# Optimization experiments

Measured on AMD Instinct MI355X. Metric: run time of the kernel, lower is better.

Reference implementation:

```python
import jax, jax.numpy as jnp
import numpy as np

DIM = 768
NUM_HEADS = 12
HEAD_DIM = DIM // NUM_HEADS
SCALE = HEAD_DIM ** -0.5
B, N = 4, 2048


def setup_inputs() -> dict:
    key = jax.random.key(0)
    k1, k2, k3 = jax.random.split(key, 3)
    x = jax.random.normal(k1, (B, N, DIM), dtype=jnp.float32)
    W_qk = jax.random.normal(k2, (2 * DIM, DIM), dtype=jnp.float32) * (DIM ** -0.5)
    b_qk = jax.random.normal(k3, (2 * DIM,), dtype=jnp.float32) * 0.02
    return {"x": x, "W_qk": W_qk, "b_qk": b_qk}


def reference(x, W_qk, b_qk):
    Bb, Nn, C = x.shape
    # qk projection: [B,N,2C] -> [B,N,2,H,D] -> q,k each [B,H,N,D]
    qk = x @ W_qk.T + b_qk
    qk = qk.reshape(Bb, Nn, 2, NUM_HEADS, HEAD_DIM).transpose(2, 0, 3, 1, 4)
    q, k = qk[0], qk[1]
    # attention scores [B,H,N,N]
    attn = jnp.einsum("bhnd,bhmd->bhnm", q, k) * SCALE
    attn = jax.nn.softmax(attn, axis=-1)
    # mean over heads, then per-query diagonal -> [B,N]
    attn_weights = jnp.diagonal(attn.mean(axis=1), axis1=-2, axis2=-1)
    return attn_weights
```

## Files before the change

### kernel.cpp

```cpp
#include <hip/hip_runtime.h>
#include <math.h>


#define B_ 4
#define N_ 2048
#define H_ 12
#define D_ 64
#define C_ 768
#define TWO_C 1536
#define QSCALE 0.18033688011112043f

typedef _Float16 half8 __attribute__((ext_vector_type(8)));
typedef _Float16 half4 __attribute__((ext_vector_type(4)));
typedef float floatx4 __attribute__((ext_vector_type(4)));

#if __has_builtin(__builtin_amdgcn_exp2f)
#define EXP2(x) __builtin_amdgcn_exp2f(x)
#else
#define EXP2(x) exp2f(x)
#endif

__device__ __forceinline__ void gload_lds16(const _Float16* g, _Float16* l) {
  __builtin_amdgcn_global_load_lds(
      (const __attribute__((address_space(1))) void*)g,
      (__attribute__((address_space(3))) void*)l, 16, 0, 0);
}

#define NX4 1572864
#define NW4 294912
__global__ __launch_bounds__(256) void conv_kernel(const float* __restrict__ x,
                                                   const float* __restrict__ W,
                                                   _Float16* __restrict__ xh,
                                                   _Float16* __restrict__ wh,
                                                   float* __restrict__ outz) {
  int i = blockIdx.x * 256 + threadIdx.x;
  if (i < 2048) {
    float4 z; z.x = 0.f; z.y = 0.f; z.z = 0.f; z.w = 0.f;
    ((float4*)outz)[i] = z;
  }
  const float* in;
  _Float16* out;
  int idx;
  if (i < NX4) {
    in = x; out = xh; idx = i;
  } else if (i < NX4 + NW4) {
    in = W; out = wh; idx = i - NX4;
  } else {
    return;
  }
  float4 v = ((const float4*)in)[idx];
  half4 o;
  o[0] = (_Float16)v.x; o[1] = (_Float16)v.y;
  o[2] = (_Float16)v.z; o[3] = (_Float16)v.w;
  ((half4*)out)[idx] = o;
}

__global__ __launch_bounds__(256) void proj_kernel(
    const _Float16* __restrict__ xh, const _Float16* __restrict__ wh,
    const float* __restrict__ bias, _Float16* __restrict__ qh,
    _Float16* __restrict__ kh) {
  __shared__ _Float16 As[3][128 * 32];
  __shared__ _Float16 Bs[3][128 * 32];
  const int t = threadIdx.x;
  const int l = t & 63;
  const int w = t >> 6;
  const int wr = w >> 1, wc = w & 1;

  int lin = blockIdx.y * 12 + blockIdx.x;
  int swz = (lin & 7) * 96 + (lin >> 3);
  const int bm = (swz / 12) * 128;
  const int bc = (swz % 12) * 128;

  const int srow = l >> 2;
  const int schunk = (l & 3) ^ ((l >> 3) & 3);

  floatx4 acc[4][4] = {};

#define PSTAGE(KT)                                                          \
  {                                                                         \
    const int sl_ = (KT) % 3;                                               \
    const int k0_ = (KT) * 32;                                              \
    _Pragma("unroll") for (int i_ = 0; i_ < 2; ++i_) {                      \
      int rb_ = w * 32 + i_ * 16;                                           \
      gload_lds16(xh + (size_t)(bm + rb_ + srow) * C_ + k0_ + schunk * 8,   \
                  As[sl_] + rb_ * 32);                                      \
      gload_lds16(wh + (size_t)(bc + rb_ + srow) * C_ + k0_ + schunk * 8,   \
                  Bs[sl_] + rb_ * 32);                                      \
    }                                                                       \
  }

#define PITER(KT, VMASM, DO_STAGE)                                          \
  {                                                                         \
    asm volatile(VMASM ::: "memory");                                       \
    __builtin_amdgcn_s_barrier();                                           \
    asm volatile("" ::: "memory");                                          \
    const int sl_ = (KT) % 3;                                               \
    const _Float16* Ap_ = As[sl_];                                          \
    const _Float16* Bp_ = Bs[sl_];                                          \
    half8 af[4], bf[4];                                                     \
    _Pragma("unroll") for (int fr = 0; fr < 4; ++fr) {                      \
      int row = wr * 64 + fr * 16 + (l & 15);                               \
      int ch = (l >> 4) ^ ((row >> 1) & 3);                                 \
      af[fr] = *(const half8*)(Ap_ + row * 32 + ch * 8);                    \
    }                                                                       \
    _Pragma("unroll") for (int fc = 0; fc < 4; ++fc) {                      \
      int row = wc * 64 + fc * 16 + (l & 15);                               \
      int ch = (l >> 4) ^ ((row >> 1) & 3);                                 \
      bf[fc] = *(const half8*)(Bp_ + row * 32 + ch * 8);                    \
    }                                                                       \
    if (DO_STAGE) PSTAGE((KT) + 2);                                         \
    _Pragma("unroll") for (int fr = 0; fr < 4; ++fr)                        \
        _Pragma("unroll") for (int fc = 0; fc < 4; ++fc) acc[fr][fc] =      \
        __builtin_amdgcn_mfma_f32_16x16x32_f16(af[fr], bf[fc],              \
                                               acc[fr][fc], 0, 0, 0);       \
  }

  PSTAGE(0);
  PSTAGE(1);
  for (int kt = 0; kt < 22; ++kt) PITER(kt, "s_waitcnt vmcnt(4)", true);
  PITER(22, "s_waitcnt vmcnt(4)", false);
  PITER(23, "s_waitcnt vmcnt(0)", false);
#undef PITER
#undef PSTAGE

#pragma unroll
  for (int fr = 0; fr < 4; ++fr) {
#pragma unroll
    for (int fc = 0; fc < 4; ++fc) {
#pragma unroll
      for (int j = 0; j < 4; ++j) {
        int m = bm + wr * 64 + fr * 16 + ((l >> 4) << 2) + j;
        int c = bc + wc * 64 + fc * 16 + (l & 15);
        float v = acc[fr][fc][j] + bias[c];
        int b = m >> 11, n = m & (N_ - 1);
        int cc = (c < C_) ? c : c - C_;
        if (c < C_) v *= QSCALE;
        int hh = cc >> 6, d = cc & 63;
        _Float16* dst = (c < C_) ? qh : kh;
        dst[((((size_t)b * H_ + hh) * N_ + n) << 6) + d] = (_Float16)v;
      }
    }
  }
}

__global__ __launch_bounds__(256) void attn_kernel(
    const _Float16* __restrict__ qh, const _Float16* __restrict__ kh,
    float* __restrict__ out) {
  __shared__ _Float16 ks[4][64 * 64];
  const int t = threadIdx.x;
  const int l = t & 63;
  const int w = t >> 6;

  int lin = blockIdx.x;
  int swz = (lin & 7) * 192 + (lin >> 3);
  const int qt = swz & 31;
  const int h = (swz >> 5) % 12;
  const int b = swz / 384;

  const _Float16* qb = qh + (((size_t)(b * H_ + h) * N_ + qt * 64) << 6);
  const _Float16* kb = kh + (((size_t)(b * H_ + h) * N_) << 6);

  half8 qf[4][2];
#pragma unroll
  for (int fr = 0; fr < 4; ++fr)
#pragma unroll
    for (int kd = 0; kd < 2; ++kd)
      qf[fr][kd] = *(const half8*)(qb + (size_t)(fr * 16 + (l & 15)) * 64 +
                                   kd * 32 + (l >> 4) * 8);

  const int lin0 = w * 64 + l;
  const int row0 = lin0 >> 3, slot0 = lin0 & 7;
  const int soff0 = row0 * 64 + (slot0 ^ (row0 & 7)) * 8;
  const int lin1 = lin0 + 256;
  const int row1 = lin1 >> 3, slot1 = lin1 & 7;
  const int soff1 = row1 * 64 + (slot1 ^ (row1 & 7)) * 8;

#define STAGE(KT)                                                   \
  {                                                                 \
    const _Float16* kp_ = kb + (size_t)(KT) * 4096;                 \
    _Float16* ld_ = ks[(KT) & 3];                                   \
    gload_lds16(kp_ + soff0, ld_ + w * 512);                        \
    gload_lds16(kp_ + soff1, ld_ + w * 512 + 2048);                 \
  }

  const int frow = w * 16 + (l & 15);
  const int koff0 = frow * 64 + (((l >> 4) + 0) ^ (l & 7)) * 8;
  const int koff1 = frow * 64 + (((l >> 4) + 4) ^ (l & 7)) * 8;

  floatx4 lsum[4] = {};
  float ed[4] = {0.f, 0.f, 0.f, 0.f};

  STAGE(0);
  STAGE(1);
  STAGE(2);

#define ITER(KT, VMASM, DO_STAGE)                                             \
  {                                                                           \
    asm volatile(VMASM ::: "memory");                                         \
    __builtin_amdgcn_s_barrier();                                             \
    asm volatile("" ::: "memory");                                            \
    const _Float16* bufp = ks[(KT) & 3];                                      \
    half8 kf0 = *(const half8*)(bufp + koff0);                                \
    half8 kf1 = *(const half8*)(bufp + koff1);                                \
    if (DO_STAGE) STAGE((KT) + 3);                                            \
    floatx4 acc[4] = {};                                                      \
    _Pragma("unroll") for (int fr = 0; fr < 4; ++fr) {                        \
      acc[fr] = __builtin_amdgcn_mfma_f32_16x16x32_f16(qf[fr][0], kf0,        \
                                                       acc[fr], 0, 0, 0);     \
      acc[fr] = __builtin_amdgcn_mfma_f32_16x16x32_f16(qf[fr][1], kf1,        \
                                                       acc[fr], 0, 0, 0);     \
    }                                                                         \
    _Pragma("unroll") for (int fr = 0; fr < 4; ++fr) {                        \
      floatx4 ev;                                                             \
      _Pragma("unroll") for (int j = 0; j < 4; ++j) ev[j] = EXP2(acc[fr][j]); \
      lsum[fr] += ev;                          \
    }                                                                         \
    if ((KT) == qt) {                                                         \
      _Pragma("unroll") for (int fr = 0; fr < 4; ++fr)                        \
          _Pragma("unroll") for (int j = 0; j < 4; ++j) {                     \
        if (fr == w && (l & 15) == (((l >> 4) << 2) + j))                     \
          ed[j] = EXP2(acc[fr][j]);                                           \
      }                                                                       \
    }                                                                         \
  }

  for (int kt = 0; kt < 29; ++kt) ITER(kt, "s_waitcnt vmcnt(4)", true);
  ITER(29, "s_waitcnt vmcnt(4)", false);
  ITER(30, "s_waitcnt vmcnt(2)", false);
  ITER(31, "s_waitcnt vmcnt(0)", false);
#undef ITER
#undef STAGE

#pragma unroll
  for (int fr = 0; fr < 4; ++fr)
#pragma unroll
    for (int j = 0; j < 4; ++j)
#pragma unroll
      for (int m = 1; m < 16; m <<= 1)
        lsum[fr][j] += __shfl_xor(lsum[fr][j], m, 16);
#pragma unroll
  for (int j = 0; j < 4; ++j)
#pragma unroll
    for (int m = 1; m < 16; m <<= 1) ed[j] += __shfl_xor(ed[j], m, 16);

  __builtin_amdgcn_s_barrier();
  float* red = (float*)ks[0];
  float* edl = red + 256;
  if ((l & 15) == 0) {
#pragma unroll
    for (int fr = 0; fr < 4; ++fr)
#pragma unroll
      for (int j = 0; j < 4; ++j)
        red[w * 64 + fr * 16 + ((l >> 4) << 2) + j] = lsum[fr][j];
#pragma unroll
    for (int j = 0; j < 4; ++j) edl[w * 16 + ((l >> 4) << 2) + j] = ed[j];
  }
  __syncthreads();

  if (t < 64) {
    float ls = red[t] + red[64 + t] + red[128 + t] + red[192 + t];
    atomicAdd(out + (size_t)b * N_ + qt * 64 + t,
              edl[t] / ls * (1.0f / (float)H_));
  }
}

extern "C" void kernel_launch(void* const* d_in, const int* in_sizes, int n_in,
                              void* d_out, int out_size, void* d_ws,
                              size_t ws_size, hipStream_t stream) {
  const float* x = (const float*)d_in[0];
  const float* W = (const float*)d_in[1];
  const float* bias = (const float*)d_in[2];
  float* out = (float*)d_out;

  char* ws = (char*)d_ws;
  _Float16* xh = (_Float16*)ws;
  _Float16* wh = (_Float16*)(ws + 12582912);
  _Float16* qh = (_Float16*)(ws + 14942208);
  _Float16* kh = (_Float16*)(ws + 27525120);

  conv_kernel<<<(NX4 + NW4 + 255) / 256, 256, 0, stream>>>(x, W, xh, wh, out);
  proj_kernel<<<dim3(TWO_C / 128, 8192 / 128), 256, 0, stream>>>(xh, wh, bias,
                                                                 qh, kh);
  attn_kernel<<<N_ / 64 * H_ * B_, 256, 0, stream>>>(qh, kh, out);
}
```

Baseline: 81.70 us.

## Split key-tile loop across two wave groups in 512-thread attention blocks

The attention kernel now runs 8 waves per block instead of 4. Each pipeline step stages a pair of 64-row K tiles, and waves 0-3 and 4-7 each take one tile of the pair, so the serial loop drops from 32 steps to 16 and there are half as many barriers per tile. The row-sum reduction now combines partials from all 8 waves, and only the wave group that holds the diagonal tile writes the diagonal exponentials. In exchange, Q fragments are loaded twice per block, LDS per block doubles to 64KB, and the barrier before reusing the staging buffer for the reduction is removed.

```diff
diff --git a/kernel.cpp b/kernel.cpp
--- a/kernel.cpp
+++ b/kernel.cpp
@@ -143,13 +143,15 @@
   }
 }
 
-__global__ __launch_bounds__(256) void attn_kernel(
+__global__ __launch_bounds__(512) void attn_kernel(
     const _Float16* __restrict__ qh, const _Float16* __restrict__ kh,
     float* __restrict__ out) {
-  __shared__ _Float16 ks[4][64 * 64];
+  __shared__ _Float16 ks[4][2][4096];
   const int t = threadIdx.x;
   const int l = t & 63;
   const int w = t >> 6;
+  const int wg = w & 3;
+  const int ts = w >> 2;
 
   int lin = blockIdx.x;
   int swz = (lin & 7) * 192 + (lin >> 3);
@@ -168,41 +170,34 @@
       qf[fr][kd] = *(const half8*)(qb + (size_t)(fr * 16 + (l & 15)) * 64 +
                                    kd * 32 + (l >> 4) * 8);
 
-  const int lin0 = w * 64 + l;
-  const int row0 = lin0 >> 3, slot0 = lin0 & 7;
-  const int soff0 = row0 * 64 + (slot0 ^ (row0 & 7)) * 8;
-  const int lin1 = lin0 + 256;
-  const int row1 = lin1 >> 3, slot1 = lin1 & 7;
-  const int soff1 = row1 * 64 + (slot1 ^ (row1 & 7)) * 8;
-
-#define STAGE(KT)                                                   \
-  {                                                                 \
-    const _Float16* kp_ = kb + (size_t)(KT) * 4096;                 \
-    _Float16* ld_ = ks[(KT) & 3];                                   \
-    gload_lds16(kp_ + soff0, ld_ + w * 512);                        \
-    gload_lds16(kp_ + soff1, ld_ + w * 512 + 2048);                 \
-  }
-
-  const int frow = w * 16 + (l & 15);
+  const int srow = t >> 3, sslot = t & 7;
+  const int soff = srow * 64 + (sslot ^ (srow & 7)) * 8;
+
+#define SPAIR(PM)                                                      \
+  {                                                                    \
+    const _Float16* kp_ = kb + (size_t)(PM) * 8192;                    \
+    gload_lds16(kp_ + soff, &ks[(PM) & 3][0][w * 512]);                \
+    gload_lds16(kp_ + 4096 + soff, &ks[(PM) & 3][1][w * 512]);         \
+  }
+
+  const int frow = wg * 16 + (l & 15);
   const int koff0 = frow * 64 + (((l >> 4) + 0) ^ (l & 7)) * 8;
   const int koff1 = frow * 64 + (((l >> 4) + 4) ^ (l & 7)) * 8;
 
   floatx4 lsum[4] = {};
   float ed[4] = {0.f, 0.f, 0.f, 0.f};
-
-  STAGE(0);
-  STAGE(1);
-  STAGE(2);
-
-#define ITER(KT, VMASM, DO_STAGE)                                             \
+  const int pm_diag = qt >> 1;
+  const bool diag_side = (ts == (qt & 1));
+
+#define ITER(PM, VMASM, DO_STAGE)                                             \
   {                                                                           \
     asm volatile(VMASM ::: "memory");                                         \
     __builtin_amdgcn_s_barrier();                                             \
     asm volatile("" ::: "memory");                                            \
-    const _Float16* bufp = ks[(KT) & 3];                                      \
+    const _Float16* bufp = &ks[(PM) & 3][ts][0];                              \
     half8 kf0 = *(const half8*)(bufp + koff0);                                \
     half8 kf1 = *(const half8*)(bufp + koff1);                                \
-    if (DO_STAGE) STAGE((KT) + 3);                                            \
+    if (DO_STAGE) SPAIR((PM) + 3);                                            \
     floatx4 acc[4] = {};                                                      \
     _Pragma("unroll") for (int fr = 0; fr < 4; ++fr) {                        \
       acc[fr] = __builtin_amdgcn_mfma_f32_16x16x32_f16(qf[fr][0], kf0,        \
@@ -213,23 +208,27 @@
     _Pragma("unroll") for (int fr = 0; fr < 4; ++fr) {                        \
       floatx4 ev;                                                             \
       _Pragma("unroll") for (int j = 0; j < 4; ++j) ev[j] = EXP2(acc[fr][j]); \
-      lsum[fr] += ev;                          \
+      lsum[fr] += ev;                                                         \
     }                                                                         \
-    if ((KT) == qt) {                                                         \
+    if ((PM) == pm_diag && diag_side) {                                       \
       _Pragma("unroll") for (int fr = 0; fr < 4; ++fr)                        \
           _Pragma("unroll") for (int j = 0; j < 4; ++j) {                     \
-        if (fr == w && (l & 15) == (((l >> 4) << 2) + j))                     \
+        if (fr == wg && (l & 15) == (((l >> 4) << 2) + j))                    \
           ed[j] = EXP2(acc[fr][j]);                                           \
       }                                                                       \
     }                                                                         \
   }
 
-  for (int kt = 0; kt < 29; ++kt) ITER(kt, "s_waitcnt vmcnt(4)", true);
-  ITER(29, "s_waitcnt vmcnt(4)", false);
-  ITER(30, "s_waitcnt vmcnt(2)", false);
-  ITER(31, "s_waitcnt vmcnt(0)", false);
+  SPAIR(0);
+  SPAIR(1);
+  SPAIR(2);
+
+  for (int pm = 0; pm < 13; ++pm) ITER(pm, "s_waitcnt vmcnt(4)", true);
+  ITER(13, "s_waitcnt vmcnt(4)", false);
+  ITER(14, "s_waitcnt vmcnt(2)", false);
+  ITER(15, "s_waitcnt vmcnt(0)", false);
 #undef ITER
-#undef STAGE
+#undef SPAIR
 
 #pragma unroll
   for (int fr = 0; fr < 4; ++fr)
@@ -243,22 +242,25 @@
 #pragma unroll
     for (int m = 1; m < 16; m <<= 1) ed[j] += __shfl_xor(ed[j], m, 16);
 
-  __builtin_amdgcn_s_barrier();
-  float* red = (float*)ks[0];
-  float* edl = red + 256;
+  float* red = (float*)&ks[0][0][0];
+  float* edl = red + 512;
   if ((l & 15) == 0) {
 #pragma unroll
     for (int fr = 0; fr < 4; ++fr)
 #pragma unroll
       for (int j = 0; j < 4; ++j)
         red[w * 64 + fr * 16 + ((l >> 4) << 2) + j] = lsum[fr][j];
-#pragma unroll
-    for (int j = 0; j < 4; ++j) edl[w * 16 + ((l >> 4) << 2) + j] = ed[j];
+    if (diag_side) {
+#pragma unroll
+      for (int j = 0; j < 4; ++j) edl[wg * 16 + ((l >> 4) << 2) + j] = ed[j];
+    }
   }
   __syncthreads();
 
   if (t < 64) {
-    float ls = red[t] + red[64 + t] + red[128 + t] + red[192 + t];
+    float ls = 0.f;
+#pragma unroll
+    for (int i = 0; i < 8; ++i) ls += red[i * 64 + t];
     atomicAdd(out + (size_t)b * N_ + qt * 64 + t,
               edl[t] / ls * (1.0f / (float)H_));
   }
@@ -281,5 +283,5 @@
   conv_kernel<<<(NX4 + NW4 + 255) / 256, 256, 0, stream>>>(x, W, xh, wh, out);
   proj_kernel<<<dim3(TWO_C / 128, 8192 / 128), 256, 0, stream>>>(xh, wh, bias,
                                                                  qh, kh);
-  attn_kernel<<<N_ / 64 * H_ * B_, 256, 0, stream>>>(qh, kh, out);
-}
+  attn_kernel<<<N_ / 64 * H_ * B_, 512, 0, stream>>>(qh, kh, out);
+}
```

Result: slower. 119.2 us (+45.9%).
